# Performance work log

Measured on AMD Instinct MI355X. Metric: run time of the kernel, lower is better.

## Reference

```python
import jax, jax.numpy as jnp
import numpy as np
import math

NUM_HEADS = 8
DIM = 512
HEAD_DIM = DIM // NUM_HEADS
SCALE = HEAD_DIM ** -0.5
RP = 2            # remove_pad = kernel_size//2 * 2 for kernel_size=3
EPS_GN = 1e-5     # GroupNorm eps
EPS_L1 = 1e-12    # F.normalize eps


def _conv(x, w, b):
    # x: [B, Cin, H, W], w: [Cout, Cin, 3, 3] (OIHW), VALID padding, stride 1
    y = jax.lax.conv_general_dilated(x, w, (1, 1), 'VALID',
                                     dimension_numbers=('NCHW', 'OIHW', 'NCHW'))
    return y + b[None, :, None, None]


def _gn_per_channel(x, g, b):
    # GroupNorm with num_groups == num_channels: per-channel norm over (H, W)
    mu = x.mean(axis=(-2, -1), keepdims=True)
    var = x.var(axis=(-2, -1), keepdims=True)
    xn = (x - mu) * jax.lax.rsqrt(var + EPS_GN)
    return xn * g[None, :, None, None] + b[None, :, None, None]


def _ppe(rpe, c1w, c1b, g1w, g1b, c2w, c2b, g2w, g2b):
    # PeripheralPositionEncoding: rpe [side^2, side^2, 4*H] -> [1, H, N, N], N=(side-2*RP)^2
    nr, _, d = rpe.shape
    side = int(round(math.sqrt(nr)))
    s2 = side - 2 * RP
    x = rpe.reshape(side, side, side, side, d)          # i j k l d
    x = x[RP:side - RP, RP:side - RP]                   # trim i, j borders
    x = x.transpose(0, 1, 4, 2, 3).reshape(s2 * s2, d, side, side)  # (ij) d k l
    x = jax.nn.relu(_gn_per_channel(_conv(x, c1w, c1b), g1w, g1b))
    x = _gn_per_channel(_conv(x, c2w, c2b), g2w, g2b)   # [(ij), H, s2, s2]
    y = x.reshape(s2 * s2, NUM_HEADS, s2 * s2).transpose(1, 0, 2)[None]  # [1,H,N,N]
    return jax.nn.sigmoid(y)


def setup_inputs() -> dict:
    key = jax.random.key(0)
    ks = jax.random.split(key, 12)
    B, N = 8, 1024            # N = (36 - 4)^2
    side = 36
    cin = NUM_HEADS * 4       # 32
    inp = {
        'x': jax.random.normal(ks[0], (B, N, DIM), jnp.float32),
        'rpe_embed': jax.random.normal(ks[1], (side * side, side * side, cin), jnp.float32),
        'wqkv': jax.random.normal(ks[2], (3 * DIM, DIM), jnp.float32) * 0.02,
        'wproj': jax.random.normal(ks[3], (DIM, DIM), jnp.float32) * 0.02,
        'bproj': jnp.zeros((DIM,), jnp.float32),
        'c1w': jax.random.normal(ks[4], (cin, cin, 3, 3), jnp.float32) * 0.02,
        'c1b': jnp.zeros((cin,), jnp.float32),
        'g1w': jnp.ones((cin,), jnp.float32),
        'g1b': jnp.zeros((cin,), jnp.float32),
        'c2w': jax.random.normal(ks[5], (NUM_HEADS, cin, 3, 3), jnp.float32) * 0.02,
        'c2b': jnp.zeros((NUM_HEADS,), jnp.float32),
        'g2w': jnp.ones((NUM_HEADS,), jnp.float32),        # norm_init[1] = 1.0
        'g2b': jnp.zeros((NUM_HEADS,), jnp.float32),       # norm_init[0] = 0.0
    }
    return inp


def reference(x, rpe_embed, wqkv, wproj, bproj, c1w, c1b, g1w, g1b, c2w, c2b, g2w, g2b):
    B, N, D = x.shape
    H, HD = NUM_HEADS, HEAD_DIM
    qkv = x @ wqkv.T                                   # [B, N, 3D]
    q, k, v = jnp.split(qkv, 3, axis=-1)
    def heads(t):
        return t.reshape(B, N, H, HD).transpose(0, 2, 1, 3)  # [B, H, N, HD]
    q, k, v = heads(q), heads(k), heads(v)
    dots = jnp.einsum('bhnd,bhmd->bhnm', q, k) * SCALE
    dots = jnp.exp(dots - dots.max(axis=-1, keepdims=True))  # stable exp-score
    w = _ppe(rpe_embed, c1w, c1b, g1w, g1b, c2w, c2b, g2w, g2b)  # [1,H,N,N]
    attn = w * dots
    attn = attn / jnp.maximum(jnp.abs(attn).sum(axis=-1, keepdims=True), EPS_L1)  # L1 normalize
    out = jnp.einsum('bhnm,bhmd->bhnd', attn, v)
    out = out.transpose(0, 2, 1, 3).reshape(B, N, D)
    return out @ wproj.T + bproj
```

## Files before the change

kernel.cpp:

```cpp
#include <hip/hip_runtime.h>
#include <hip/hip_fp16.h>


typedef __attribute__((ext_vector_type(8))) short bf16x8;
typedef __attribute__((ext_vector_type(8))) _Float16 f16x8;
typedef __attribute__((ext_vector_type(4))) float f32x4;

__device__ __forceinline__ unsigned short f2bf(float f) {
  unsigned u = __builtin_bit_cast(unsigned, f);
  u += 0x7FFFu + ((u >> 16) & 1u);
  return (unsigned short)(u >> 16);
}

template<bool OUT_BF16>
__global__ __launch_bounds__(256) void gemm_f16_bt(
    const float* __restrict__ A, const float* __restrict__ B,
    void* __restrict__ Cv, const float* __restrict__ bias,
    int M, int N, int K)
{
  __shared__ __align__(16) _Float16 As[128 * 40];
  __shared__ __align__(16) _Float16 Bs[128 * 40];
  const int tid = threadIdx.x;
  const int wv = tid >> 6, ln = tid & 63, lr = ln & 15, lq = ln >> 4;
  const int wm = wv >> 1, wn = wv & 1;
  const int m0 = blockIdx.y * 128, n0 = blockIdx.x * 128;

  f32x4 acc[4][4];
#pragma unroll
  for (int i = 0; i < 4; i++)
#pragma unroll
    for (int j = 0; j < 4; j++) acc[i][j] = (f32x4){0.f, 0.f, 0.f, 0.f};

  const int sr = tid >> 1, sk = (tid & 1) * 16;
  const float* Ap = A + (size_t)(m0 + sr) * K + sk;
  const float* Bp = B + (size_t)(n0 + sr) * K + sk;

  for (int k0 = 0; k0 < K; k0 += 32) {
    float4 av0 = *(const float4*)(Ap + k0);
    float4 av1 = *(const float4*)(Ap + k0 + 4);
    float4 av2 = *(const float4*)(Ap + k0 + 8);
    float4 av3 = *(const float4*)(Ap + k0 + 12);
    float4 bv0 = *(const float4*)(Bp + k0);
    float4 bv1 = *(const float4*)(Bp + k0 + 4);
    float4 bv2 = *(const float4*)(Bp + k0 + 8);
    float4 bv3 = *(const float4*)(Bp + k0 + 12);
    __syncthreads();
    {
      f16x8 p0, p1, r0, r1;
      p0[0]=(_Float16)av0.x; p0[1]=(_Float16)av0.y; p0[2]=(_Float16)av0.z; p0[3]=(_Float16)av0.w;
      p0[4]=(_Float16)av1.x; p0[5]=(_Float16)av1.y; p0[6]=(_Float16)av1.z; p0[7]=(_Float16)av1.w;
      p1[0]=(_Float16)av2.x; p1[1]=(_Float16)av2.y; p1[2]=(_Float16)av2.z; p1[3]=(_Float16)av2.w;
      p1[4]=(_Float16)av3.x; p1[5]=(_Float16)av3.y; p1[6]=(_Float16)av3.z; p1[7]=(_Float16)av3.w;
      r0[0]=(_Float16)bv0.x; r0[1]=(_Float16)bv0.y; r0[2]=(_Float16)bv0.z; r0[3]=(_Float16)bv0.w;
      r0[4]=(_Float16)bv1.x; r0[5]=(_Float16)bv1.y; r0[6]=(_Float16)bv1.z; r0[7]=(_Float16)bv1.w;
      r1[0]=(_Float16)bv2.x; r1[1]=(_Float16)bv2.y; r1[2]=(_Float16)bv2.z; r1[3]=(_Float16)bv2.w;
      r1[4]=(_Float16)bv3.x; r1[5]=(_Float16)bv3.y; r1[6]=(_Float16)bv3.z; r1[7]=(_Float16)bv3.w;
      *(f16x8*)&As[sr * 40 + sk] = p0;
      *(f16x8*)&As[sr * 40 + sk + 8] = p1;
      *(f16x8*)&Bs[sr * 40 + sk] = r0;
      *(f16x8*)&Bs[sr * 40 + sk + 8] = r1;
    }
    __syncthreads();
    f16x8 af[4], bf[4];
#pragma unroll
    for (int mf = 0; mf < 4; mf++)
      af[mf] = *(const f16x8*)&As[(wm * 64 + mf * 16 + lr) * 40 + lq * 8];
#pragma unroll
    for (int nf = 0; nf < 4; nf++)
      bf[nf] = *(const f16x8*)&Bs[(wn * 64 + nf * 16 + lr) * 40 + lq * 8];
#pragma unroll
    for (int mf = 0; mf < 4; mf++)
#pragma unroll
      for (int nf = 0; nf < 4; nf++)
        acc[mf][nf] = __builtin_amdgcn_mfma_f32_16x16x32_f16(af[mf], bf[nf], acc[mf][nf], 0, 0, 0);
  }

#pragma unroll
  for (int mf = 0; mf < 4; mf++)
#pragma unroll
    for (int reg = 0; reg < 4; reg++) {
      const int row = m0 + wm * 64 + mf * 16 + lq * 4 + reg;
#pragma unroll
      for (int nf = 0; nf < 4; nf++) {
        const int col = n0 + wn * 64 + nf * 16 + lr;
        float v = acc[mf][nf][reg];
        if (bias) v += bias[col];
        if (OUT_BF16) ((unsigned short*)Cv)[(size_t)row * N + col] = f2bf(v);
        else          ((float*)Cv)[(size_t)row * N + col] = v;
      }
    }
}

__global__ __launch_bounds__(512, 1) void conv_fused(
    const float* __restrict__ rpe,
    const float* __restrict__ c1w, const float* __restrict__ g1, const float* __restrict__ b1,
    const float* __restrict__ c2w, const float* __restrict__ g2, const float* __restrict__ b2,
    float* __restrict__ wout)
{
  extern __shared__ __align__(16) char smem[];
  unsigned short* inA = (unsigned short*)smem;
  unsigned short* yB  = (unsigned short*)(smem + 82944);
  unsigned short* wH1 = yB;
  unsigned short* wH2 = yB + 9216;
  float* statL = (float*)(smem + 156928);
  float* aL    = (float*)(smem + 158976);
  float* cL    = aL + 32;
  float* transF = (float*)smem;

  const int tid = threadIdx.x;
  const int wv = tid >> 6, ln = tid & 63;
  const int lr = ln & 15, lq = ln >> 4;
  const int p = blockIdx.x;

  const float* src = rpe + (size_t)(((p >> 5) + 2) * 36 + (p & 31) + 2) * 41472;
  for (int t = tid; t < 10368; t += 512) {
    int pix = t >> 3, dq = (t & 7) << 2;
    float4 v = *(const float4*)(src + pix * 32 + dq);
    __half2 h0 = __floats2half2_rn(v.x, v.y);
    __half2 h1 = __floats2half2_rn(v.z, v.w);
    uint2 u; u.x = __builtin_bit_cast(unsigned, h0); u.y = __builtin_bit_cast(unsigned, h1);
    *(uint2*)(inA + pix * 32 + dq) = u;
  }
  for (int t = tid; t < 9216; t += 512) {
    int oc = t / 288, rem = t - oc * 288;
    int ic = rem / 9, tap = rem - ic * 9;
    wH1[(tap * 32 + oc) * 32 + ic] = __half_as_ushort(__float2half(c1w[t]));
  }
  for (int t = tid; t < 2304; t += 512) {
    int oc = t / 288, rem = t - oc * 288;
    int ic = rem / 9, tap = rem - ic * 9;
    wH2[(tap * 8 + oc) * 32 + ic] = __half_as_ushort(__float2half(c2w[t]));
  }
  __syncthreads();

  f16x8 w1f[2][9];
  const int ic0 = lq * 8;
#pragma unroll
  for (int ct = 0; ct < 2; ct++) {
    int oc = 2 * lr + ct;
#pragma unroll
    for (int tap = 0; tap < 9; tap++)
      w1f[ct][tap] = *(const f16x8*)&wH1[(tap * 32 + oc) * 32 + ic0];
  }
  f16x8 w2f[9];
#pragma unroll
  for (int tap = 0; tap < 9; tap++) {
    if (lr < 8) w2f[tap] = *(const f16x8*)&wH2[(tap * 8 + lr) * 32 + ic0];
    else {
      f16x8 z;
#pragma unroll
      for (int j = 0; j < 8; j++) z[j] = (_Float16)0.f;
      w2f[tap] = z;
    }
  }
  __syncthreads();

  constexpr int OFF1[9] = {0, 32, 64, 1152, 1184, 1216, 2304, 2336, 2368};
  float s0 = 0.f, q0 = 0.f, s1 = 0.f, q1 = 0.f;
  for (int t = wv; t < 73; t += 8) {
    int m = t * 16 + lr;
    int ms = m < 1155 ? m : 1155;
    const unsigned short* ab = inA + ((ms / 34) * 36 + (ms % 34)) * 32 + lq * 8;
    f32x4 c0 = {0.f, 0.f, 0.f, 0.f}, c1v = {0.f, 0.f, 0.f, 0.f};
#pragma unroll
    for (int tap = 0; tap < 9; tap++) {
      f16x8 av = *(const f16x8*)(ab + OFF1[tap]);
      c0  = __builtin_amdgcn_mfma_f32_16x16x32_f16(av, w1f[0][tap], c0, 0, 0, 0);
      c1v = __builtin_amdgcn_mfma_f32_16x16x32_f16(av, w1f[1][tap], c1v, 0, 0, 0);
    }
#pragma unroll
    for (int r = 0; r < 4; r++) {
      int mo = t * 16 + lq * 4 + r;
      if (mo < 1156) {
        float v0 = c0[r], v1 = c1v[r];
        unsigned u = (unsigned)__half_as_ushort(__float2half(v0))
                   | ((unsigned)__half_as_ushort(__float2half(v1)) << 16);
        *(unsigned*)&yB[mo * 32 + lr * 2] = u;
        s0 += v0; q0 += v0 * v0; s1 += v1; q1 += v1 * v1;
      }
    }
  }
#pragma unroll
  for (int off = 16; off < 64; off <<= 1) {
    s0 += __shfl_xor(s0, off); q0 += __shfl_xor(q0, off);
    s1 += __shfl_xor(s1, off); q1 += __shfl_xor(q1, off);
  }
  if (ln < 16) {
    float* st = statL + wv * 64;
    st[ln] = s0; st[16 + ln] = q0; st[32 + ln] = s1; st[48 + ln] = q1;
  }
  __syncthreads();
  if (tid < 32) {
    int cti = tid >> 4, lri = tid & 15;
    float s = 0.f, q = 0.f;
#pragma unroll
    for (int w = 0; w < 8; w++) {
      s += statL[w * 64 + cti * 32 + lri];
      q += statL[w * 64 + cti * 32 + 16 + lri];
    }
    int ch = 2 * lri + cti;
    float mu = s * (1.f / 1156.f);
    float var = q * (1.f / 1156.f) - mu * mu;
    float a_ = rsqrtf(var + 1e-5f) * g1[ch];
    aL[ch] = a_; cL[ch] = b1[ch] - mu * a_;
  }
  __syncthreads();

  for (int i = tid * 8; i < 36992; i += 4096) {
    f16x8 raw = *(const f16x8*)(yB + i);
    int ocb = i & 31;
    f16x8 outv;
#pragma unroll
    for (int e = 0; e < 8; e++) {
      float v = (float)raw[e];
      v = fmaxf(v * aL[ocb + e] + cL[ocb + e], 0.f);
      outv[e] = (_Float16)v;
    }
    *(f16x8*)(yB + i) = outv;
  }
  __syncthreads();

  constexpr int OFF2[9] = {0, 32, 64, 1088, 1120, 1152, 2176, 2208, 2240};
  float s2 = 0.f, q2 = 0.f;
  for (int t = wv; t < 64; t += 8) {
    int m = t * 16 + lr;
    const unsigned short* ab = yB + ((m >> 5) * 34 + (m & 31)) * 32 + lq * 8;
    f32x4 cc = {0.f, 0.f, 0.f, 0.f};
#pragma unroll
    for (int tap = 0; tap < 9; tap++) {
      f16x8 av = *(const f16x8*)(ab + OFF2[tap]);
      cc = __builtin_amdgcn_mfma_f32_16x16x32_f16(av, w2f[tap], cc, 0, 0, 0);
    }
#pragma unroll
    for (int r = 0; r < 4; r++) {
      int mo = t * 16 + lq * 4 + r;
      float v = cc[r];
      s2 += v; q2 += v * v;
      if (lr < 8) transF[lr * 1032 + mo] = v;
    }
  }
#pragma unroll
  for (int off = 16; off < 64; off <<= 1) {
    s2 += __shfl_xor(s2, off); q2 += __shfl_xor(q2, off);
  }
  if (ln < 16) { statL[wv * 32 + ln] = s2; statL[wv * 32 + 16 + ln] = q2; }
  __syncthreads();
  if (tid < 8) {
    float s = 0.f, q = 0.f;
#pragma unroll
    for (int w = 0; w < 8; w++) { s += statL[w * 32 + tid]; q += statL[w * 32 + 16 + tid]; }
    float mu = s * (1.f / 1024.f);
    float var = q * (1.f / 1024.f) - mu * mu;
    float a_ = rsqrtf(var + 1e-5f) * g2[tid];
    aL[tid] = a_; cL[tid] = b2[tid] - mu * a_;
  }
  __syncthreads();

  for (int idx = tid; idx < 2048; idx += 512) {
    int oc = idx >> 8, p4 = (idx & 255) << 2;
    float4 v = *(const float4*)&transF[oc * 1032 + p4];
    float a_ = aL[oc], c_ = cL[oc];
    float4 o;
    o.x = 1.f / (1.f + __expf(-(v.x * a_ + c_)));
    o.y = 1.f / (1.f + __expf(-(v.y * a_ + c_)));
    o.z = 1.f / (1.f + __expf(-(v.z * a_ + c_)));
    o.w = 1.f / (1.f + __expf(-(v.w * a_ + c_)));
    *(float4*)(wout + ((size_t)oc << 20) + ((size_t)p << 10) + p4) = o;
  }
}

__global__ __launch_bounds__(256) void attn_kernel(
    const unsigned short* __restrict__ qkv,
    const float* __restrict__ wppe,
    float* __restrict__ oh)
{
  __shared__ __align__(16) unsigned short k_lds[64 * 72];
  __shared__ __align__(16) unsigned short v_lds[64 * 72];
  __shared__ __align__(16) unsigned short p_lds[4 * 16 * 72];
  const int tid = threadIdx.x;
  const int wv = tid >> 6, ln = tid & 63;
  const int lr = ln & 15, lq = ln >> 4;
  const int b = blockIdx.y >> 3, h = blockIdx.y & 7;
  const int n0 = blockIdx.x << 6;

  const size_t qoff = (size_t)((b << 10) + n0 + (wv << 4) + lr) * 1536 + (h << 6);
  bf16x8 qf0 = *(const bf16x8*)(qkv + qoff + lq * 8);
  bf16x8 qf1 = *(const bf16x8*)(qkv + qoff + 32 + lq * 8);

  f32x4 acc[4];
#pragma unroll
  for (int dt = 0; dt < 4; dt++) acc[dt] = (f32x4){0.f, 0.f, 0.f, 0.f};
  float den[4] = {0.f, 0.f, 0.f, 0.f};
  const float* wp = wppe + ((size_t)h << 20);

  for (int m0 = 0; m0 < 1024; m0 += 64) {
    __syncthreads();
    for (int t = tid; t < 512; t += 256) {
      int m = t >> 3, dq = t & 7;
      const unsigned short* kr = qkv + (size_t)((b << 10) + m0 + m) * 1536 + 512 + (h << 6) + dq * 8;
      *(uint4*)&k_lds[m * 72 + dq * 8] = *(const uint4*)kr;
      uint4 vvv = *(const uint4*)(kr + 512);
      unsigned short tmp[8];
      *(uint4*)tmp = vvv;
#pragma unroll
      for (int i = 0; i < 8; i++) {
        int d = dq * 8 + i;
        v_lds[d * 72 + (m ^ (((d >> 3) & 7) << 3))] = tmp[i];
      }
    }
    __syncthreads();

    f32x4 s[4];
#pragma unroll
    for (int mt = 0; mt < 4; mt++) {
      const unsigned short* kb = &k_lds[(mt * 16 + lr) * 72 + lq * 8];
      f32x4 cz = (f32x4){0.f, 0.f, 0.f, 0.f};
      cz = __builtin_amdgcn_mfma_f32_16x16x32_bf16(qf0, *(const bf16x8*)kb, cz, 0, 0, 0);
      cz = __builtin_amdgcn_mfma_f32_16x16x32_bf16(qf1, *(const bf16x8*)(kb + 32), cz, 0, 0, 0);
      s[mt] = cz;
    }
#pragma unroll
    for (int mt = 0; mt < 4; mt++)
#pragma unroll
      for (int reg = 0; reg < 4; reg++) {
        int rrow = lq * 4 + reg;
        float wvl = wp[(size_t)(n0 + (wv << 4) + rrow) * 1024 + (m0 + mt * 16 + lr)];
        float pv = wvl * __expf(s[mt][reg] * 0.125f);
        den[reg] += pv;
        p_lds[((wv << 4) + rrow) * 72 + mt * 16 + lr] = f2bf(pv);
      }
    const unsigned short* pb = &p_lds[((wv << 4) + lr) * 72];
    bf16x8 pa0 = *(const bf16x8*)(pb + lq * 8);
    bf16x8 pa1 = *(const bf16x8*)(pb + 32 + lq * 8);
#pragma unroll
    for (int dt = 0; dt < 4; dt++) {
      int d = dt * 16 + lr;
      int sw = ((d >> 3) & 7) << 3;
      const unsigned short* vb = &v_lds[d * 72];
      acc[dt] = __builtin_amdgcn_mfma_f32_16x16x32_bf16(pa0, *(const bf16x8*)(vb + ((lq * 8) ^ sw)), acc[dt], 0, 0, 0);
      acc[dt] = __builtin_amdgcn_mfma_f32_16x16x32_bf16(pa1, *(const bf16x8*)(vb + ((32 + lq * 8) ^ sw)), acc[dt], 0, 0, 0);
    }
  }
#pragma unroll
  for (int off = 1; off < 16; off <<= 1)
#pragma unroll
    for (int reg = 0; reg < 4; reg++) den[reg] += __shfl_xor(den[reg], off);
#pragma unroll
  for (int dt = 0; dt < 4; dt++)
#pragma unroll
    for (int reg = 0; reg < 4; reg++) {
      size_t row = (size_t)((b << 10) + n0 + (wv << 4) + lq * 4 + reg);
      oh[row * 512 + (h << 6) + dt * 16 + lr] = acc[dt][reg] / den[reg];
    }
}

extern "C" void kernel_launch(void* const* d_in, const int* in_sizes, int n_in,
                              void* d_out, int out_size, void* d_ws, size_t ws_size,
                              hipStream_t stream) {
  (void)in_sizes; (void)n_in; (void)out_size; (void)ws_size;
  const float* x     = (const float*)d_in[0];
  const float* rpe   = (const float*)d_in[1];
  const float* wqkv  = (const float*)d_in[2];
  const float* wproj = (const float*)d_in[3];
  const float* bproj = (const float*)d_in[4];
  const float* c1w   = (const float*)d_in[5];
  const float* g1w   = (const float*)d_in[7];
  const float* g1b   = (const float*)d_in[8];
  const float* c2w   = (const float*)d_in[9];
  const float* g2w   = (const float*)d_in[11];
  const float* g2b   = (const float*)d_in[12];
  float* out = (float*)d_out;

  char* ws = (char*)d_ws;
  unsigned short* qkv_bf = (unsigned short*)ws;
  float* wppe = (float*)(ws + 25165824);
  float* ohb  = (float*)(ws + 58720256);

  gemm_f16_bt<true><<<dim3(12, 64), 256, 0, stream>>>(x, wqkv, qkv_bf, nullptr, 8192, 1536, 512);

  const int ldsC = 159232;
  hipFuncSetAttribute(reinterpret_cast<const void*>(&conv_fused),
                      hipFuncAttributeMaxDynamicSharedMemorySize, ldsC);
  conv_fused<<<1024, 512, ldsC, stream>>>(rpe, c1w, g1w, g1b, c2w, g2w, g2b, wppe);

  attn_kernel<<<dim3(16, 64), 256, 0, stream>>>(qkv_bf, wppe, ohb);

  gemm_f16_bt<false><<<dim3(4, 64), 256, 0, stream>>>(ohb, wproj, out, bproj, 8192, 512, 512);
}
```

Before: 222.3 us.

## Double conv block threads and switch LDS to channel-group-planar layout

The fused PPE conv kernel now runs 1024 threads per block instead of 512, halving per-wave work in the loads and both conv loops. The input and intermediate LDS buffers move from pixel-interleaved 32-channel rows to four planar groups of 8 channels, which changes the bank access pattern of the MFMA operand reads. GroupNorm statistics are reduced with LDS atomics instead of per-wave slots. Second-conv weights are read from LDS inside the tap loop rather than held in registers, which lowers register pressure for the larger block but adds LDS traffic.

```diff
diff --git a/kernel.cpp b/kernel.cpp
--- a/kernel.cpp
+++ b/kernel.cpp
@@ -91,7 +91,7 @@
     }
 }
 
-__global__ __launch_bounds__(512, 1) void conv_fused(
+__global__ __launch_bounds__(1024, 1) void conv_fused(
     const float* __restrict__ rpe,
     const float* __restrict__ c1w, const float* __restrict__ g1, const float* __restrict__ b1,
     const float* __restrict__ c2w, const float* __restrict__ g2, const float* __restrict__ b2,
@@ -101,9 +101,9 @@
   unsigned short* inA = (unsigned short*)smem;
   unsigned short* yB  = (unsigned short*)(smem + 82944);
   unsigned short* wH1 = yB;
-  unsigned short* wH2 = yB + 9216;
-  float* statL = (float*)(smem + 156928);
-  float* aL    = (float*)(smem + 158976);
+  unsigned short* wH2 = (unsigned short*)(smem + 156928);
+  float* statA = (float*)(smem + 161536);
+  float* aL    = (float*)(smem + 161792);
   float* cL    = aL + 32;
   float* transF = (float*)smem;
 
@@ -112,21 +112,23 @@
   const int lr = ln & 15, lq = ln >> 4;
   const int p = blockIdx.x;
 
+  if (tid < 64) statA[tid] = 0.f;
+
   const float* src = rpe + (size_t)(((p >> 5) + 2) * 36 + (p & 31) + 2) * 41472;
-  for (int t = tid; t < 10368; t += 512) {
+  for (int t = tid; t < 10368; t += 1024) {
     int pix = t >> 3, dq = (t & 7) << 2;
     float4 v = *(const float4*)(src + pix * 32 + dq);
     __half2 h0 = __floats2half2_rn(v.x, v.y);
     __half2 h1 = __floats2half2_rn(v.z, v.w);
     uint2 u; u.x = __builtin_bit_cast(unsigned, h0); u.y = __builtin_bit_cast(unsigned, h1);
-    *(uint2*)(inA + pix * 32 + dq) = u;
-  }
-  for (int t = tid; t < 9216; t += 512) {
+    *(uint2*)&inA[(dq >> 3) * 10368 + pix * 8 + (dq & 7)] = u;
+  }
+  for (int t = tid; t < 9216; t += 1024) {
     int oc = t / 288, rem = t - oc * 288;
     int ic = rem / 9, tap = rem - ic * 9;
     wH1[(tap * 32 + oc) * 32 + ic] = __half_as_ushort(__float2half(c1w[t]));
   }
-  for (int t = tid; t < 2304; t += 512) {
+  for (int t = tid; t < 2304; t += 1024) {
     int oc = t / 288, rem = t - oc * 288;
     int ic = rem / 9, tap = rem - ic * 9;
     wH2[(tap * 8 + oc) * 32 + ic] = __half_as_ushort(__float2half(c2w[t]));
@@ -142,25 +144,15 @@
     for (int tap = 0; tap < 9; tap++)
       w1f[ct][tap] = *(const f16x8*)&wH1[(tap * 32 + oc) * 32 + ic0];
   }
-  f16x8 w2f[9];
-#pragma unroll
-  for (int tap = 0; tap < 9; tap++) {
-    if (lr < 8) w2f[tap] = *(const f16x8*)&wH2[(tap * 8 + lr) * 32 + ic0];
-    else {
-      f16x8 z;
-#pragma unroll
-      for (int j = 0; j < 8; j++) z[j] = (_Float16)0.f;
-      w2f[tap] = z;
-    }
-  }
-  __syncthreads();
-
-  constexpr int OFF1[9] = {0, 32, 64, 1152, 1184, 1216, 2304, 2336, 2368};
+  __syncthreads();
+
+  constexpr int OFF1[9] = {0, 8, 16, 288, 296, 304, 576, 584, 592};
   float s0 = 0.f, q0 = 0.f, s1 = 0.f, q1 = 0.f;
-  for (int t = wv; t < 73; t += 8) {
+  const unsigned short* inAg = inA + lq * 10368;
+  for (int t = wv; t < 73; t += 16) {
     int m = t * 16 + lr;
     int ms = m < 1155 ? m : 1155;
-    const unsigned short* ab = inA + ((ms / 34) * 36 + (ms % 34)) * 32 + lq * 8;
+    const unsigned short* ab = inAg + ((ms / 34) * 36 + (ms % 34)) * 8;
     f32x4 c0 = {0.f, 0.f, 0.f, 0.f}, c1v = {0.f, 0.f, 0.f, 0.f};
 #pragma unroll
     for (int tap = 0; tap < 9; tap++) {
@@ -175,7 +167,7 @@
         float v0 = c0[r], v1 = c1v[r];
         unsigned u = (unsigned)__half_as_ushort(__float2half(v0))
                    | ((unsigned)__half_as_ushort(__float2half(v1)) << 16);
-        *(unsigned*)&yB[mo * 32 + lr * 2] = u;
+        *(unsigned*)&yB[(lr >> 2) * 9248 + mo * 8 + ((lr * 2) & 7)] = u;
         s0 += v0; q0 += v0 * v0; s1 += v1; q1 += v1 * v1;
       }
     }
@@ -186,69 +178,71 @@
     s1 += __shfl_xor(s1, off); q1 += __shfl_xor(q1, off);
   }
   if (ln < 16) {
-    float* st = statL + wv * 64;
-    st[ln] = s0; st[16 + ln] = q0; st[32 + ln] = s1; st[48 + ln] = q1;
+    atomicAdd(&statA[ln], s0);      atomicAdd(&statA[16 + ln], q0);
+    atomicAdd(&statA[32 + ln], s1); atomicAdd(&statA[48 + ln], q1);
   }
   __syncthreads();
   if (tid < 32) {
     int cti = tid >> 4, lri = tid & 15;
-    float s = 0.f, q = 0.f;
-#pragma unroll
-    for (int w = 0; w < 8; w++) {
-      s += statL[w * 64 + cti * 32 + lri];
-      q += statL[w * 64 + cti * 32 + 16 + lri];
-    }
+    float s = statA[cti * 32 + lri];
+    float q = statA[cti * 32 + 16 + lri];
     int ch = 2 * lri + cti;
     float mu = s * (1.f / 1156.f);
     float var = q * (1.f / 1156.f) - mu * mu;
     float a_ = rsqrtf(var + 1e-5f) * g1[ch];
     aL[ch] = a_; cL[ch] = b1[ch] - mu * a_;
   }
-  __syncthreads();
-
-  for (int i = tid * 8; i < 36992; i += 4096) {
-    f16x8 raw = *(const f16x8*)(yB + i);
-    int ocb = i & 31;
-    f16x8 outv;
-#pragma unroll
-    for (int e = 0; e < 8; e++) {
-      float v = (float)raw[e];
-      v = fmaxf(v * aL[ocb + e] + cL[ocb + e], 0.f);
-      outv[e] = (_Float16)v;
-    }
-    *(f16x8*)(yB + i) = outv;
-  }
-  __syncthreads();
-
-  constexpr int OFF2[9] = {0, 32, 64, 1088, 1120, 1152, 2176, 2208, 2240};
+  if (tid < 16) statA[tid] = 0.f;
+  __syncthreads();
+
+  {
+    int g = tid >> 8, ocb = g * 8;
+    unsigned short* yg = yB + g * 9248;
+    for (int pix = (tid & 255); pix < 1156; pix += 256) {
+      f16x8 raw = *(const f16x8*)&yg[pix * 8];
+      f16x8 outv;
+#pragma unroll
+      for (int e = 0; e < 8; e++) {
+        float v = (float)raw[e];
+        v = fmaxf(v * aL[ocb + e] + cL[ocb + e], 0.f);
+        outv[e] = (_Float16)v;
+      }
+      *(f16x8*)&yg[pix * 8] = outv;
+    }
+  }
+  __syncthreads();
+
+  constexpr int OFF2[9] = {0, 8, 16, 272, 280, 288, 544, 552, 560};
+  const unsigned short* yBg = yB + lq * 9248;
   float s2 = 0.f, q2 = 0.f;
-  for (int t = wv; t < 64; t += 8) {
+  for (int t = wv; t < 64; t += 16) {
     int m = t * 16 + lr;
-    const unsigned short* ab = yB + ((m >> 5) * 34 + (m & 31)) * 32 + lq * 8;
+    const unsigned short* ab = yBg + ((m >> 5) * 34 + (m & 31)) * 8;
     f32x4 cc = {0.f, 0.f, 0.f, 0.f};
 #pragma unroll
     for (int tap = 0; tap < 9; tap++) {
       f16x8 av = *(const f16x8*)(ab + OFF2[tap]);
-      cc = __builtin_amdgcn_mfma_f32_16x16x32_f16(av, w2f[tap], cc, 0, 0, 0);
+      f16x8 wf = *(const f16x8*)&wH2[(tap * 8 + (lr & 7)) * 32 + ic0];
+      cc = __builtin_amdgcn_mfma_f32_16x16x32_f16(av, wf, cc, 0, 0, 0);
     }
 #pragma unroll
     for (int r = 0; r < 4; r++) {
       int mo = t * 16 + lq * 4 + r;
       float v = cc[r];
-      s2 += v; q2 += v * v;
-      if (lr < 8) transF[lr * 1032 + mo] = v;
+      if (lr < 8) {
+        s2 += v; q2 += v * v;
+        transF[lr * 1032 + mo] = v;
+      }
     }
   }
 #pragma unroll
   for (int off = 16; off < 64; off <<= 1) {
     s2 += __shfl_xor(s2, off); q2 += __shfl_xor(q2, off);
   }
-  if (ln < 16) { statL[wv * 32 + ln] = s2; statL[wv * 32 + 16 + ln] = q2; }
+  if (ln < 8) { atomicAdd(&statA[ln], s2); atomicAdd(&statA[8 + ln], q2); }
   __syncthreads();
   if (tid < 8) {
-    float s = 0.f, q = 0.f;
-#pragma unroll
-    for (int w = 0; w < 8; w++) { s += statL[w * 32 + tid]; q += statL[w * 32 + 16 + tid]; }
+    float s = statA[tid], q = statA[8 + tid];
     float mu = s * (1.f / 1024.f);
     float var = q * (1.f / 1024.f) - mu * mu;
     float a_ = rsqrtf(var + 1e-5f) * g2[tid];
@@ -256,7 +250,7 @@
   }
   __syncthreads();
 
-  for (int idx = tid; idx < 2048; idx += 512) {
+  for (int idx = tid; idx < 2048; idx += 1024) {
     int oc = idx >> 8, p4 = (idx & 255) << 2;
     float4 v = *(const float4*)&transF[oc * 1032 + p4];
     float a_ = aL[oc], c_ = cL[oc];
@@ -378,10 +372,10 @@
 
   gemm_f16_bt<true><<<dim3(12, 64), 256, 0, stream>>>(x, wqkv, qkv_bf, nullptr, 8192, 1536, 512);
 
-  const int ldsC = 159232;
+  const int ldsC = 162048;
   hipFuncSetAttribute(reinterpret_cast<const void*>(&conv_fused),
                       hipFuncAttributeMaxDynamicSharedMemorySize, ldsC);
-  conv_fused<<<1024, 512, ldsC, stream>>>(rpe, c1w, g1w, g1b, c2w, g2w, g2b, wppe);
+  conv_fused<<<1024, 1024, ldsC, stream>>>(rpe, c1w, g1w, g1b, c2w, g2w, g2b, wppe);
 
   attn_kernel<<<dim3(16, 64), 256, 0, stream>>>(qkv_bf, wppe, ohb);
 
```

Measured after the change: 217.8 us. -2.0%, faster.
